# Kernel optimization log

Hardware: AMD Instinct MI355X
Metric: run time of the kernel (lower is better)

The kernel has to match this reference:

```python
import jax, jax.numpy as jnp
import numpy as np

BS, SEQ, ENC, DEC, HEADS, INTERM = 32, 2048, 512, 512, 8, 128
IH = INTERM * HEADS


def setup_inputs() -> dict:
    key = jax.random.key(0)
    ks = jax.random.split(key, 16)
    s = 0.02
    return {
        "enc": jax.random.normal(ks[0], (BS, SEQ, ENC), jnp.float32),
        "dec": jax.random.normal(ks[1], (BS, 1, DEC + ENC), jnp.float32),
        "kappa": jax.random.uniform(ks[2], (BS, 1, HEADS), jnp.float32),
        "mask": jnp.ones((BS, SEQ, 1), jnp.float32),
        "Wv": jax.random.normal(ks[3], (ENC, IH), jnp.float32) * s,
        "bv": jnp.zeros((IH,), jnp.float32),
        "Wq": jax.random.normal(ks[4], (DEC + ENC, IH), jnp.float32) * s,
        "bq": jnp.zeros((IH,), jnp.float32),
        "Wf": jax.random.normal(ks[5], (IH, HEADS), jnp.float32) * s,
        "bf": jnp.zeros((HEADS,), jnp.float32),
        "Wb": jax.random.normal(ks[6], (DEC + ENC, HEADS), jnp.float32) * s,
        "bb": jnp.zeros((HEADS,), jnp.float32),
        "Wk": jax.random.normal(ks[7], (DEC + ENC, HEADS), jnp.float32) * s,
        "bk": jnp.zeros((HEADS,), jnp.float32),
        "Wfc": jax.random.normal(ks[8], (ENC * HEADS, ENC), jnp.float32) * s,
        "bfc": jnp.zeros((ENC,), jnp.float32),
    }


def reference(enc, dec, kappa, mask, Wv, bv, Wq, bq, Wf, bf, Wb, bb, Wk, bk, Wfc, bfc):
    bs, seq_len, _ = enc.shape
    sp = jax.nn.softplus
    value = enc @ Wv + bv                      # (bs, seq, IH)
    query = dec @ Wq + bq                      # (bs, 1, IH), broadcasts over seq
    alpha = sp(jnp.tanh(query + value) @ Wf + bf) * mask   # (bs, seq, heads)
    beta = sp(dec @ Wb + bb)                   # (bs, 1, heads)
    kappa = kappa + sp(dec @ Wk + bk)          # (bs, 1, heads)
    u = jnp.arange(seq_len, dtype=enc.dtype)[None, :, None]
    score = alpha * jnp.exp(-beta * (kappa - u) ** 2)       # (bs, seq, heads)
    # weighted reduction over seq: (bs, heads, enc) then flatten in heads-major order
    context = jnp.einsum("bsh,bse->bhe", score, enc).reshape(bs, -1)
    context = context @ Wfc + bfc              # (bs, enc)
    return context[:, None, :], kappa, score
```

## Files before the change

kernel.cpp:

```cpp
#include <hip/hip_runtime.h>
#include <cstdint>
#include <cstddef>

#define BSZ    32
#define SEQL   2048
#define ENCD   512
#define DE     1024
#define NHEADS 8
#define IHD    1024

typedef unsigned short u16;
typedef __bf16 bf16x8 __attribute__((ext_vector_type(8)));
typedef float floatx4 __attribute__((ext_vector_type(4)));
typedef unsigned short u16x8 __attribute__((ext_vector_type(8)));

__device__ __forceinline__ u16 f2bf(float f) {
    unsigned int u = __float_as_uint(f);
    u = (u + 0x7FFFu + ((u >> 16) & 1u)) >> 16;
    return (u16)u;
}
__device__ __forceinline__ float bf2f(u16 v) {
    return __uint_as_float(((unsigned int)v) << 16);
}
__device__ __forceinline__ float softplus_f(float x) {
    return fmaxf(x, 0.0f) + log1pf(__expf(-fabsf(x)));
}
__device__ __forceinline__ float tanh_fast(float x) {
    const float e = __expf(2.0f * x);
    return 1.0f - 2.0f / (e + 1.0f);
}
__device__ __forceinline__ void async_cp16(u16* lds, const u16* g) {
    __builtin_amdgcn_global_load_lds(
        (const __attribute__((address_space(1))) unsigned int*)g,
        (__attribute__((address_space(3))) unsigned int*)lds, 16, 0, 0);
}

__global__ __launch_bounds__(256) void pre_kernel(
    const float* __restrict__ Wv, const float* __restrict__ Wf,
    u16* __restrict__ WvT, u16* __restrict__ wfb,
    const float* __restrict__ dec, const float* __restrict__ kappa_in,
    const float* __restrict__ Wq, const float* __restrict__ bq,
    const float* __restrict__ bv,
    const float* __restrict__ Wb, const float* __restrict__ bb,
    const float* __restrict__ Wk, const float* __restrict__ bk,
    float* __restrict__ query_ws, float* __restrict__ beta_ws,
    float* __restrict__ kappa_out)
{
    __shared__ float sh[64 * 65];
    const int bid = blockIdx.x, tid = threadIdx.x;

    if (bid < 128) {
        const int nt = bid & 15, kt = bid >> 4;
        for (int i = tid; i < 4096; i += 256) {
            const int kk = i >> 6, nn = i & 63;
            sh[kk * 65 + nn] = Wv[(size_t)(kt * 64 + kk) * IHD + nt * 64 + nn];
        }
        __syncthreads();
        for (int i = tid; i < 4096; i += 256) {
            const int nn = i >> 6, kk = i & 63;
            WvT[(size_t)(nt * 64 + nn) * 512 + kt * 64 + kk] = f2bf(sh[kk * 65 + nn]);
        }
        return;
    }
    if (bid == 128) {
        for (int i = tid; i < 8192; i += 256) {
            const int j   = i & 7;
            const int fr8 = (i >> 3) & 7;
            const int qd  = (i >> 6) & 3;
            const int ks  = (i >> 8) & 3;
            const int nn  = i >> 10;
            const int row = nn * 128 + ks * 32 + qd * 8 + j;
            wfb[i] = f2bf(Wf[row * NHEADS + fr8]);
        }
        return;
    }
    const int p = bid - 129;
    const int b = p & 31, y = p >> 5;
    float* s_dec = sh;
    float* s_red = sh + DE;
    for (int i = tid; i < DE; i += 256) s_dec[i] = dec[b * DE + i];
    __syncthreads();

    if (y < 32) {
        const int cl = tid & 31, kg = tid >> 5;
        const int col = y * 32 + cl;
        float a = 0.f;
        const float* w = Wq + col;
        #pragma unroll 8
        for (int k = kg * 128; k < kg * 128 + 128; ++k)
            a = fmaf(s_dec[k], w[(size_t)k * IHD], a);
        s_red[tid] = a;
        __syncthreads();
        if (tid < 32) {
            float s = 0.f;
            #pragma unroll
            for (int i = 0; i < 8; ++i) s += s_red[i * 32 + tid];
            query_ws[(size_t)b * IHD + col] = s + bq[col] + bv[col];
        }
    } else {
        const int h = tid & 7, kg = tid >> 3;
        float ab = 0.f, ak = 0.f;
        for (int k = kg * 32; k < kg * 32 + 32; ++k) {
            const float d = s_dec[k];
            ab = fmaf(d, Wb[k * NHEADS + h], ab);
            ak = fmaf(d, Wk[k * NHEADS + h], ak);
        }
        s_red[tid] = ab;
        __syncthreads();
        for (int off = 128; off >= 8; off >>= 1) {
            if (tid < off) s_red[tid] += s_red[tid + off];
            __syncthreads();
        }
        const float abT = (tid < 8) ? s_red[tid] : 0.f;
        __syncthreads();
        s_red[tid] = ak;
        __syncthreads();
        for (int off = 128; off >= 8; off >>= 1) {
            if (tid < off) s_red[tid] += s_red[tid + off];
            __syncthreads();
        }
        if (tid < 8) {
            beta_ws[b * NHEADS + tid]   = softplus_f(bb[tid] + abT);
            kappa_out[b * NHEADS + tid] = kappa_in[b * NHEADS + tid]
                                        + softplus_f(bk[tid] + s_red[tid]);
        }
    }
}

#define BM 128

__global__ __launch_bounds__(256, 2) void gemm_score_ctx_kernel(
    const float* __restrict__ enc, u16* __restrict__ encb,
    const u16* __restrict__ wvT,
    const u16* __restrict__ wfb2, const float* __restrict__ bf_g,
    const float* __restrict__ mask, const float* __restrict__ query_ws,
    const float* __restrict__ beta_ws, const float* __restrict__ kappa_out,
    float* __restrict__ score_out, float* __restrict__ ctx_part)
{
    __shared__ __align__(16) unsigned char smem[69632];
    u16*   tT      = (u16*)(smem + 32768);
    float* s_score = (float*)(smem + 65536);

    const int tid  = threadIdx.x;
    const int m0   = blockIdx.x * BM;
    const int b    = blockIdx.x >> 4;
    const int sc   = blockIdx.x & 15;
    const int lane = tid & 63;
    const int w    = tid >> 6;
    const int wr   = w >> 1, wc = w & 1;
    const int fr   = lane & 15, quad = lane >> 4;

    {
        const float4* src = (const float4*)enc + (size_t)m0 * 128;
        u16x8* dst = (u16x8*)(encb + (size_t)m0 * 512);
        for (int base = 0; base < 32; base += 8) {
            float4 av[8], bw[8];
            #pragma unroll
            for (int u = 0; u < 8; ++u) {
                const int i = (base + u) * 256 + tid;
                av[u] = src[i * 2];
                bw[u] = src[i * 2 + 1];
            }
            #pragma unroll
            for (int u = 0; u < 8; ++u) {
                const int i = (base + u) * 256 + tid;
                u16x8 o;
                o[0] = f2bf(av[u].x); o[1] = f2bf(av[u].y);
                o[2] = f2bf(av[u].z); o[3] = f2bf(av[u].w);
                o[4] = f2bf(bw[u].x); o[5] = f2bf(bw[u].y);
                o[6] = f2bf(bw[u].z); o[7] = f2bf(bw[u].w);
                dst[i] = o;
            }
        }
        asm volatile("s_waitcnt vmcnt(0)" ::: "memory");
        __builtin_amdgcn_sched_barrier(0);
        __builtin_amdgcn_s_barrier();
    }

    int mA[4], csA[4];
    #pragma unroll
    for (int r = 0; r < 4; ++r) {
        const int c = r * 256 + tid;
        mA[r]  = c >> 3;
        csA[r] = (c & 7) ^ (mA[r] & 7);
    }

    auto stage = [&](int bufsel, int it) {
        u16* Ab = (u16*)(smem + bufsel * 32768);
        u16* Bb = Ab + 8192;
        const int nn2 = it >> 3, kt2 = it & 7;
        const size_t aoff = (size_t)kt2 * 64;
        const size_t boff = (size_t)nn2 * (128 * 512) + (size_t)kt2 * 64;
        #pragma unroll
        for (int r = 0; r < 4; ++r) {
            async_cp16(Ab + (r * 256 + (tid & 192)) * 8,
                       encb + (size_t)(m0 + mA[r]) * 512 + aoff + csA[r] * 8);
            async_cp16(Bb + (size_t)(r * 256 + (tid & 192)) * 8,
                       wvT + (size_t)mA[r] * 512 + boff + csA[r] * 8);
        }
    };

    floatx4 acc2[2] = {};

    stage(0, 0);

    for (int nn = 0; nn < 8; ++nn) {
        const int n0 = nn * 128;
        float qv[4];
        bf16x8 wfr[4];
        floatx4 acc[4][4] = {};

        #pragma unroll
        for (int kt = 0; kt < 8; ++kt) {
            const int it = nn * 8 + kt;
            if (kt < 7 || nn < 7)
                stage((it + 1) & 1, it + 1);
            if (kt == 0) {
                #pragma unroll
                for (int nt = 0; nt < 4; ++nt)
                    qv[nt] = query_ws[(size_t)b * IHD + n0 + wc * 64 + nt * 16 + fr];
                #pragma unroll
                for (int ks = 0; ks < 4; ++ks)
                    wfr[ks] = *(const bf16x8*)&wfb2[((nn * 4 + ks) * 4 + quad) * 64
                                                    + (fr & 7) * 8];
            }
            if (kt == 7 && nn == 7) {
                asm volatile("s_waitcnt vmcnt(0)" ::: "memory");
            } else if (kt == 0) {
                asm volatile("s_waitcnt vmcnt(16)" ::: "memory");
            } else {
                asm volatile("s_waitcnt vmcnt(8)" ::: "memory");
            }
            __builtin_amdgcn_sched_barrier(0);
            __builtin_amdgcn_s_barrier();

            u16* Ab = (u16*)(smem + (it & 1) * 32768);
            u16* Bb = Ab + 8192;
            __builtin_amdgcn_s_setprio(1);
            #pragma unroll
            for (int s2 = 0; s2 < 2; ++s2) {
                bf16x8 af[4], bfr[4];
                #pragma unroll
                for (int mt = 0; mt < 4; ++mt) {
                    const int ma = wr * 64 + mt * 16 + fr;
                    const int ca = (s2 * 4 + quad) ^ (ma & 7);
                    af[mt] = *(const bf16x8*)&Ab[ma * 64 + ca * 8];
                }
                #pragma unroll
                for (int nt = 0; nt < 4; ++nt) {
                    const int nb = wc * 64 + nt * 16 + fr;
                    const int cb = (s2 * 4 + quad) ^ (nb & 7);
                    bfr[nt] = *(const bf16x8*)&Bb[nb * 64 + cb * 8];
                }
                #pragma unroll
                for (int mt = 0; mt < 4; ++mt)
                    #pragma unroll
                    for (int nt = 0; nt < 4; ++nt)
                        acc[mt][nt] = __builtin_amdgcn_mfma_f32_16x16x32_bf16(
                            af[mt], bfr[nt], acc[mt][nt], 0, 0, 0);
            }
            __builtin_amdgcn_s_setprio(0);
            __builtin_amdgcn_sched_barrier(0);
            __builtin_amdgcn_s_barrier();
        }

        #pragma unroll
        for (int mt = 0; mt < 4; ++mt) {
            #pragma unroll
            for (int nt = 0; nt < 4; ++nt) {
                const int col = wc * 64 + nt * 16 + fr;
                #pragma unroll
                for (int reg = 0; reg < 4; ++reg) {
                    const int row = wr * 64 + mt * 16 + quad * 4 + reg;
                    ((__bf16*)tT)[row * 128 + (col ^ ((row & 7) << 3))] =
                        (__bf16)tanh_fast(acc[mt][nt][reg] + qv[nt]);
                }
            }
        }
        asm volatile("s_waitcnt lgkmcnt(0)" ::: "memory");
        __builtin_amdgcn_sched_barrier(0);
        __builtin_amdgcn_s_barrier();

        #pragma unroll
        for (int t = 0; t < 2; ++t) {
            const int row = w * 32 + t * 16 + fr;
            #pragma unroll
            for (int ks = 0; ks < 4; ++ks) {
                const bf16x8 ta = *(const bf16x8*)
                    &tT[row * 128 + ((ks * 32 + quad * 8) ^ ((row & 7) << 3))];
                acc2[t] = __builtin_amdgcn_mfma_f32_16x16x32_bf16(ta, wfr[ks], acc2[t], 0, 0, 0);
            }
        }
        __builtin_amdgcn_sched_barrier(0);
        __builtin_amdgcn_s_barrier();
    }

    if (fr < NHEADS) {
        const float bfh = bf_g[fr];
        const float bet = beta_ws[b * NHEADS + fr];
        const float kap = kappa_out[b * NHEADS + fr];
        #pragma unroll
        for (int t = 0; t < 2; ++t) {
            #pragma unroll
            for (int reg = 0; reg < 4; ++reg) {
                const int row  = w * 32 + t * 16 + quad * 4 + reg;
                const int grow = m0 + row;
                const int s = grow & 2047;
                const float alpha = softplus_f(acc2[t][reg] + bfh) * mask[grow];
                const float du = kap - (float)s;
                s_score[row * NHEADS + fr] = alpha * __expf(-bet * du * du);
            }
        }
    }
    asm volatile("s_waitcnt lgkmcnt(0)" ::: "memory");
    __builtin_amdgcn_s_barrier();

    {
        const float4* src4 = (const float4*)s_score;
        float4* dst4 = (float4*)(score_out + (size_t)m0 * NHEADS);
        dst4[tid] = src4[tid];
    }

    {
        float acc0[8] = {}, acc1[8] = {};
        const u16* ep = encb + (size_t)m0 * 512 + lane * 8;
        for (int s0 = 0; s0 < 128; s0 += 16) {
            u16x8 ev[16];
            #pragma unroll
            for (int u = 0; u < 16; ++u)
                ev[u] = *(const u16x8*)(ep + (size_t)(s0 + u) * 512);
            #pragma unroll
            for (int u = 0; u < 16; ++u) {
                const float2 sc2 = *(const float2*)&s_score[(s0 + u) * NHEADS + 2 * w];
                #pragma unroll
                for (int j = 0; j < 8; ++j) {
                    const float e = bf2f(ev[u][j]);
                    acc0[j] = fmaf(sc2.x, e, acc0[j]);
                    acc1[j] = fmaf(sc2.y, e, acc1[j]);
                }
            }
        }
        const int e8 = lane * 8;
        float* outp = ctx_part + ((size_t)sc * BSZ + b) * (NHEADS * ENCD);
        *(float4*)&outp[(2 * w + 0) * ENCD + e8]     = make_float4(acc0[0], acc0[1], acc0[2], acc0[3]);
        *(float4*)&outp[(2 * w + 0) * ENCD + e8 + 4] = make_float4(acc0[4], acc0[5], acc0[6], acc0[7]);
        *(float4*)&outp[(2 * w + 1) * ENCD + e8]     = make_float4(acc1[0], acc1[1], acc1[2], acc1[3]);
        *(float4*)&outp[(2 * w + 1) * ENCD + e8 + 4] = make_float4(acc1[4], acc1[5], acc1[6], acc1[7]);
    }
}

__global__ __launch_bounds__(256) void ctx_reduce_kernel(
    const float* __restrict__ part, float* __restrict__ ctx_ws)
{
    const int i = blockIdx.x * 256 + threadIdx.x;
    float a = 0.f;
    #pragma unroll
    for (int sc = 0; sc < 16; ++sc)
        a += part[(size_t)sc * 131072 + i];
    ctx_ws[i] = a;
}

__global__ __launch_bounds__(256) void final_kernel(
    const float* __restrict__ ctx_ws, const float* __restrict__ Wfc,
    const float* __restrict__ bfc, float* __restrict__ out_ctx)
{
    __shared__ float s_ctx[32][128];
    const int jc = blockIdx.x, ks = blockIdx.y, tid = threadIdx.x;
    const int jl = tid & 31, bg = tid >> 5;
    const int j = jc * 32 + jl;
    const int k0 = ks * 128;

    for (int i = tid; i < 32 * 128; i += 256) {
        const int bb2 = i >> 7, kk = i & 127;
        s_ctx[bb2][kk] = ctx_ws[(size_t)bb2 * (NHEADS * ENCD) + k0 + kk];
    }
    __syncthreads();

    float a0 = 0.f, a1 = 0.f, a2 = 0.f, a3 = 0.f;
    for (int kk = 0; kk < 128; ++kk) {
        const float wv = Wfc[(size_t)(k0 + kk) * ENCD + j];
        a0 = fmaf(s_ctx[bg * 4 + 0][kk], wv, a0);
        a1 = fmaf(s_ctx[bg * 4 + 1][kk], wv, a1);
        a2 = fmaf(s_ctx[bg * 4 + 2][kk], wv, a2);
        a3 = fmaf(s_ctx[bg * 4 + 3][kk], wv, a3);
    }
    const float bias = (ks == 0) ? bfc[j] : 0.0f;
    atomicAdd(&out_ctx[(bg * 4 + 0) * ENCD + j], a0 + bias);
    atomicAdd(&out_ctx[(bg * 4 + 1) * ENCD + j], a1 + bias);
    atomicAdd(&out_ctx[(bg * 4 + 2) * ENCD + j], a2 + bias);
    atomicAdd(&out_ctx[(bg * 4 + 3) * ENCD + j], a3 + bias);
}

extern "C" void kernel_launch(void* const* d_in, const int* in_sizes, int n_in,
                              void* d_out, int out_size, void* d_ws, size_t ws_size,
                              hipStream_t stream)
{
    const float* enc   = (const float*)d_in[0];
    const float* dec   = (const float*)d_in[1];
    const float* kapin = (const float*)d_in[2];
    const float* mask  = (const float*)d_in[3];
    const float* Wv    = (const float*)d_in[4];
    const float* bv    = (const float*)d_in[5];
    const float* Wq    = (const float*)d_in[6];
    const float* bq    = (const float*)d_in[7];
    const float* Wf    = (const float*)d_in[8];
    const float* bf    = (const float*)d_in[9];
    const float* Wb    = (const float*)d_in[10];
    const float* bb    = (const float*)d_in[11];
    const float* Wk    = (const float*)d_in[12];
    const float* bk    = (const float*)d_in[13];
    const float* Wfc   = (const float*)d_in[14];
    const float* bfc   = (const float*)d_in[15];

    float* out       = (float*)d_out;
    float* out_ctx   = out;
    float* out_kappa = out + 16384;
    float* out_score = out + 16640;

    char* w = (char*)d_ws;
    u16*   enc_bf   = (u16*)w;
    float* ctx_part = (float*)(w + 67108864);
    u16*   wvT      = (u16*)(w + 75497472);
    float* q_ws     = (float*)(w + 76546048);
    float* beta_ws  = (float*)(w + 76677120);
    float* ctx_ws   = (float*)(w + 76678144);
    u16*   wfb      = (u16*)(w + 77202432);

    hipMemsetAsync(out_ctx, 0, 16384 * sizeof(float), stream);

    pre_kernel<<<dim3(128 + 1 + 1056), dim3(256), 0, stream>>>(
        Wv, Wf, wvT, wfb,
        dec, kapin, Wq, bq, bv, Wb, bb, Wk, bk, q_ws, beta_ws, out_kappa);

    gemm_score_ctx_kernel<<<dim3((BSZ * SEQL) / BM), dim3(256), 0, stream>>>(
        enc, enc_bf, wvT, wfb, bf, mask, q_ws, beta_ws, out_kappa,
        out_score, ctx_part);

    ctx_reduce_kernel<<<dim3(512), dim3(256), 0, stream>>>(ctx_part, ctx_ws);

    final_kernel<<<dim3(16, 32), dim3(256), 0, stream>>>(
        ctx_ws, Wfc, bfc, out_ctx);
}
```

Measured before the change: 393.8 us.

## Batch the query projection across the batch and split-K partials into the GEMM

```diff
diff --git a/kernel.cpp b/kernel.cpp
--- a/kernel.cpp
+++ b/kernel.cpp
@@ -39,14 +39,13 @@
     const float* __restrict__ Wv, const float* __restrict__ Wf,
     u16* __restrict__ WvT, u16* __restrict__ wfb,
     const float* __restrict__ dec, const float* __restrict__ kappa_in,
-    const float* __restrict__ Wq, const float* __restrict__ bq,
-    const float* __restrict__ bv,
+    const float* __restrict__ Wq,
     const float* __restrict__ Wb, const float* __restrict__ bb,
     const float* __restrict__ Wk, const float* __restrict__ bk,
-    float* __restrict__ query_ws, float* __restrict__ beta_ws,
+    float* __restrict__ qpart, float* __restrict__ beta_ws,
     float* __restrict__ kappa_out)
 {
-    __shared__ float sh[64 * 65];
+    __shared__ float sh[8192];
     const int bid = blockIdx.x, tid = threadIdx.x;
 
     if (bid < 128) {
@@ -75,55 +74,62 @@
         return;
     }
     const int p = bid - 129;
-    const int b = p & 31, y = p >> 5;
+    if (p < 128) {
+        const int ct = p & 31, kg = p >> 5;
+        for (int i = tid; i < 8192; i += 256) {
+            const int bb2 = i >> 8, kk = i & 255;
+            sh[i] = dec[(size_t)bb2 * DE + kg * 256 + kk];
+        }
+        __syncthreads();
+        const int cl = tid & 31, bg = tid >> 5;
+        const int col = ct * 32 + cl;
+        float a0 = 0.f, a1 = 0.f, a2 = 0.f, a3 = 0.f;
+        const float* wq = Wq + (size_t)kg * 256 * IHD + col;
+        #pragma unroll 8
+        for (int k = 0; k < 256; ++k) {
+            const float wv = wq[(size_t)k * IHD];
+            a0 = fmaf(sh[(bg * 4 + 0) * 256 + k], wv, a0);
+            a1 = fmaf(sh[(bg * 4 + 1) * 256 + k], wv, a1);
+            a2 = fmaf(sh[(bg * 4 + 2) * 256 + k], wv, a2);
+            a3 = fmaf(sh[(bg * 4 + 3) * 256 + k], wv, a3);
+        }
+        float* outp = qpart + (size_t)kg * (BSZ * IHD) + col;
+        outp[(size_t)(bg * 4 + 0) * IHD] = a0;
+        outp[(size_t)(bg * 4 + 1) * IHD] = a1;
+        outp[(size_t)(bg * 4 + 2) * IHD] = a2;
+        outp[(size_t)(bg * 4 + 3) * IHD] = a3;
+        return;
+    }
+    const int b = p - 128;
     float* s_dec = sh;
     float* s_red = sh + DE;
     for (int i = tid; i < DE; i += 256) s_dec[i] = dec[b * DE + i];
     __syncthreads();
-
-    if (y < 32) {
-        const int cl = tid & 31, kg = tid >> 5;
-        const int col = y * 32 + cl;
-        float a = 0.f;
-        const float* w = Wq + col;
-        #pragma unroll 8
-        for (int k = kg * 128; k < kg * 128 + 128; ++k)
-            a = fmaf(s_dec[k], w[(size_t)k * IHD], a);
-        s_red[tid] = a;
+    const int h = tid & 7, kg = tid >> 3;
+    float ab = 0.f, ak = 0.f;
+    for (int k = kg * 32; k < kg * 32 + 32; ++k) {
+        const float d = s_dec[k];
+        ab = fmaf(d, Wb[k * NHEADS + h], ab);
+        ak = fmaf(d, Wk[k * NHEADS + h], ak);
+    }
+    s_red[tid] = ab;
+    __syncthreads();
+    for (int off = 128; off >= 8; off >>= 1) {
+        if (tid < off) s_red[tid] += s_red[tid + off];
         __syncthreads();
-        if (tid < 32) {
-            float s = 0.f;
-            #pragma unroll
-            for (int i = 0; i < 8; ++i) s += s_red[i * 32 + tid];
-            query_ws[(size_t)b * IHD + col] = s + bq[col] + bv[col];
-        }
-    } else {
-        const int h = tid & 7, kg = tid >> 3;
-        float ab = 0.f, ak = 0.f;
-        for (int k = kg * 32; k < kg * 32 + 32; ++k) {
-            const float d = s_dec[k];
-            ab = fmaf(d, Wb[k * NHEADS + h], ab);
-            ak = fmaf(d, Wk[k * NHEADS + h], ak);
-        }
-        s_red[tid] = ab;
+    }
+    const float abT = (tid < 8) ? s_red[tid] : 0.f;
+    __syncthreads();
+    s_red[tid] = ak;
+    __syncthreads();
+    for (int off = 128; off >= 8; off >>= 1) {
+        if (tid < off) s_red[tid] += s_red[tid + off];
         __syncthreads();
-        for (int off = 128; off >= 8; off >>= 1) {
-            if (tid < off) s_red[tid] += s_red[tid + off];
-            __syncthreads();
-        }
-        const float abT = (tid < 8) ? s_red[tid] : 0.f;
-        __syncthreads();
-        s_red[tid] = ak;
-        __syncthreads();
-        for (int off = 128; off >= 8; off >>= 1) {
-            if (tid < off) s_red[tid] += s_red[tid + off];
-            __syncthreads();
-        }
-        if (tid < 8) {
-            beta_ws[b * NHEADS + tid]   = softplus_f(bb[tid] + abT);
-            kappa_out[b * NHEADS + tid] = kappa_in[b * NHEADS + tid]
-                                        + softplus_f(bk[tid] + s_red[tid]);
-        }
+    }
+    if (tid < 8) {
+        beta_ws[b * NHEADS + tid]   = softplus_f(bb[tid] + abT);
+        kappa_out[b * NHEADS + tid] = kappa_in[b * NHEADS + tid]
+                                    + softplus_f(bk[tid] + s_red[tid]);
     }
 }
 
@@ -133,7 +139,8 @@
     const float* __restrict__ enc, u16* __restrict__ encb,
     const u16* __restrict__ wvT,
     const u16* __restrict__ wfb2, const float* __restrict__ bf_g,
-    const float* __restrict__ mask, const float* __restrict__ query_ws,
+    const float* __restrict__ mask, const float* __restrict__ qpart,
+    const float* __restrict__ bq_g, const float* __restrict__ bv_g,
     const float* __restrict__ beta_ws, const float* __restrict__ kappa_out,
     float* __restrict__ score_out, float* __restrict__ ctx_part)
 {
@@ -206,8 +213,6 @@
 
     for (int nn = 0; nn < 8; ++nn) {
         const int n0 = nn * 128;
-        float qv[4];
-        bf16x8 wfr[4];
         floatx4 acc[4][4] = {};
 
         #pragma unroll
@@ -215,19 +220,8 @@
             const int it = nn * 8 + kt;
             if (kt < 7 || nn < 7)
                 stage((it + 1) & 1, it + 1);
-            if (kt == 0) {
-                #pragma unroll
-                for (int nt = 0; nt < 4; ++nt)
-                    qv[nt] = query_ws[(size_t)b * IHD + n0 + wc * 64 + nt * 16 + fr];
-                #pragma unroll
-                for (int ks = 0; ks < 4; ++ks)
-                    wfr[ks] = *(const bf16x8*)&wfb2[((nn * 4 + ks) * 4 + quad) * 64
-                                                    + (fr & 7) * 8];
-            }
             if (kt == 7 && nn == 7) {
                 asm volatile("s_waitcnt vmcnt(0)" ::: "memory");
-            } else if (kt == 0) {
-                asm volatile("s_waitcnt vmcnt(16)" ::: "memory");
             } else {
                 asm volatile("s_waitcnt vmcnt(8)" ::: "memory");
             }
@@ -264,6 +258,22 @@
             __builtin_amdgcn_s_barrier();
         }
 
+        float qv[4];
+        bf16x8 wfr[4];
+        #pragma unroll
+        for (int nt = 0; nt < 4; ++nt) {
+            const int col = n0 + wc * 64 + nt * 16 + fr;
+            float t = qpart[(size_t)b * IHD + col];
+            t += qpart[(size_t)(BSZ * IHD) * 1 + (size_t)b * IHD + col];
+            t += qpart[(size_t)(BSZ * IHD) * 2 + (size_t)b * IHD + col];
+            t += qpart[(size_t)(BSZ * IHD) * 3 + (size_t)b * IHD + col];
+            qv[nt] = (t + bq_g[col]) + bv_g[col];
+        }
+        #pragma unroll
+        for (int ks = 0; ks < 4; ++ks)
+            wfr[ks] = *(const bf16x8*)&wfb2[((nn * 4 + ks) * 4 + quad) * 64
+                                            + (fr & 7) * 8];
+
         #pragma unroll
         for (int mt = 0; mt < 4; ++mt) {
             #pragma unroll
@@ -421,19 +431,19 @@
     u16*   enc_bf   = (u16*)w;
     float* ctx_part = (float*)(w + 67108864);
     u16*   wvT      = (u16*)(w + 75497472);
-    float* q_ws     = (float*)(w + 76546048);
     float* beta_ws  = (float*)(w + 76677120);
+    float* qpart    = (float*)(w + 76678144);
     float* ctx_ws   = (float*)(w + 76678144);
     u16*   wfb      = (u16*)(w + 77202432);
 
     hipMemsetAsync(out_ctx, 0, 16384 * sizeof(float), stream);
 
-    pre_kernel<<<dim3(128 + 1 + 1056), dim3(256), 0, stream>>>(
+    pre_kernel<<<dim3(289), dim3(256), 0, stream>>>(
         Wv, Wf, wvT, wfb,
-        dec, kapin, Wq, bq, bv, Wb, bb, Wk, bk, q_ws, beta_ws, out_kappa);
+        dec, kapin, Wq, Wb, bb, Wk, bk, qpart, beta_ws, out_kappa);
 
     gemm_score_ctx_kernel<<<dim3((BSZ * SEQL) / BM), dim3(256), 0, stream>>>(
-        enc, enc_bf, wvT, wfb, bf, mask, q_ws, beta_ws, out_kappa,
+        enc, enc_bf, wvT, wfb, bf, mask, qpart, bq, bv, beta_ws, out_kappa,
         out_score, ctx_part);
 
     ctx_reduce_kernel<<<dim3(512), dim3(256), 0, stream>>>(ctx_part, ctx_ws);
```

New measurement: 409.1 us. +3.9%, slower.
